# Kernel optimization log

Measured on AMD Instinct MI355X. Metric: run time of the kernel, lower is better.

Reference implementation:

```python
import jax, jax.numpy as jnp
import numpy as np

N_NODES = 50000
N_EDGES = 300000
IN_FEATS = 1433
HIDDEN = 16
OUT_FEATS = 7


def setup_inputs() -> dict:
    key = jax.random.key(0)
    k1, k2, k3, k4, k5, k6, k7, k8 = jax.random.split(key, 8)
    features = jax.random.normal(k1, (N_NODES, IN_FEATS), dtype=jnp.float32)
    src = jax.random.randint(k2, (N_EDGES,), 0, N_NODES, dtype=jnp.int32)
    dst = jax.random.randint(k3, (N_EDGES,), 0, N_NODES, dtype=jnp.int32)
    # Linear layer params (PyTorch default-ish init scale)
    s1 = 1.0 / np.sqrt(IN_FEATS)
    s2 = 1.0 / np.sqrt(HIDDEN)
    W1 = jax.random.uniform(k4, (IN_FEATS, HIDDEN), jnp.float32, -s1, s1)
    b1 = jax.random.uniform(k5, (HIDDEN,), jnp.float32, -s1, s1)
    W2 = jax.random.uniform(k6, (HIDDEN, OUT_FEATS), jnp.float32, -s2, s2)
    b2 = jax.random.uniform(k7, (OUT_FEATS,), jnp.float32, -s2, s2)
    return {"features": features, "src": src, "dst": dst,
            "W1": W1, "b1": b1, "W2": W2, "b2": b2}


def _gcn_layer(h, src, dst, W, b):
    # copy_src message + sum reduce + self term: h'_v = sum_{u->v} h_u + h_v
    agg = jax.ops.segment_sum(h[src], dst, num_segments=N_NODES) + h
    return agg @ W + b


def reference(features, src, dst, W1, b1, W2, b2):
    x = jax.nn.relu(_gcn_layer(features, src, dst, W1, b1))
    # dropout is identity in eval mode
    x = _gcn_layer(x, src, dst, W2, b2)
    return x
```

## Files before the change

kernel.cpp:

```cpp
#include <hip/hip_runtime.h>
#include <hip/hip_fp16.h>

#define N_NODES  50000
#define N_EDGES  300000
#define IN_FEATS 1433
#define HIDDEN   16
#define OUT_F    7
#define KPAD     1472
#define WROW     9

__global__ __launch_bounds__(256) void k1_gemm(
    const float* __restrict__ F, const float* __restrict__ W1,
    const float* __restrict__ b1, __half* __restrict__ H,
    __half* __restrict__ aggbuf)
{
    __shared__ unsigned int Wl[KPAD * WROW];
    const int tid = threadIdx.x;

    for (int idx = tid; idx < KPAD * 8; idx += 256) {
        int k = idx >> 3, c = idx & 7;
        unsigned int u = 0u;
        if (k < IN_FEATS) {
            __half2 h2 = __floats2half2_rn(W1[k * 16 + 2 * c], W1[k * 16 + 2 * c + 1]);
            u = *reinterpret_cast<unsigned int*>(&h2);
        }
        Wl[k * WROW + c] = u;
    }
    __syncthreads();

    const int lane = tid & 63;
    const float b1v = b1[lane & 15];
    const int gwave  = blockIdx.x * 4 + (tid >> 6);
    const int nwaves = gridDim.x * 4;

    for (int ch = gwave; ch < N_NODES / 4; ch += nwaves) {
        const int r0 = ch * 4;
        const float* fp = F + (size_t)r0 * IN_FEATS;

        float v[64];
        #pragma unroll
        for (int i = 0; i < 64; ++i) v[i] = 0.f;

        #pragma unroll 2
        for (int i = 0; i < 22; ++i) {
            const int k = i * 64 + lane;
            const float f0 = fp[k];
            const float f1 = fp[IN_FEATS + k];
            const float f2 = fp[2 * IN_FEATS + k];
            const float f3 = fp[3 * IN_FEATS + k];
            float wv[16];
            #pragma unroll
            for (int c = 0; c < 8; ++c) {
                unsigned int u = Wl[k * WROW + c];
                __half2 h2 = *reinterpret_cast<__half2*>(&u);
                float2 f = __half22float2(h2);
                wv[2 * c]     = f.x;
                wv[2 * c + 1] = f.y;
            }
            #pragma unroll
            for (int j = 0; j < 16; ++j) {
                v[j]      += f0 * wv[j];
                v[16 + j] += f1 * wv[j];
                v[32 + j] += f2 * wv[j];
                v[48 + j] += f3 * wv[j];
            }
        }
        {
            const int k = 1408 + lane;
            float f0 = 0.f, f1 = 0.f, f2 = 0.f, f3 = 0.f;
            if (k < IN_FEATS) {
                f0 = fp[k];
                f1 = fp[IN_FEATS + k];
                f2 = fp[2 * IN_FEATS + k];
                f3 = fp[3 * IN_FEATS + k];
            }
            float wv[16];
            #pragma unroll
            for (int c = 0; c < 8; ++c) {
                unsigned int u = Wl[k * WROW + c];
                __half2 h2 = *reinterpret_cast<__half2*>(&u);
                float2 f = __half22float2(h2);
                wv[2 * c]     = f.x;
                wv[2 * c + 1] = f.y;
            }
            #pragma unroll
            for (int j = 0; j < 16; ++j) {
                v[j]      += f0 * wv[j];
                v[16 + j] += f1 * wv[j];
                v[32 + j] += f2 * wv[j];
                v[48 + j] += f3 * wv[j];
            }
        }

        #pragma unroll
        for (int d = 5; d >= 0; --d) {
            const int half = 1 << d;
            const bool hi = (lane >> d) & 1;
            #pragma unroll
            for (int t = 0; t < (1 << d); ++t) {
                float sent = hi ? v[t] : v[t + half];
                float recv = __shfl_xor(sent, half, 64);
                float keep = hi ? v[t + half] : v[t];
                v[t] = keep + recv;
            }
        }
        const size_t off = (size_t)r0 * 16 + lane;
        H[off]      = __float2half(v[0]);
        aggbuf[off] = __float2half(v[0] + b1v);
    }
}

__global__ __launch_bounds__(256) void k2_scatter1(
    const int* __restrict__ src, const int* __restrict__ dst,
    const __half2* __restrict__ H2, __half2* __restrict__ agg2)
{
    int t = blockIdx.x * 256 + threadIdx.x;
    int e = t >> 3, p = t & 7;
    int s = src[e], d = dst[e];
    __half2 val = H2[(size_t)s * 8 + p];
    unsafeAtomicAdd(&agg2[(size_t)d * 8 + p], val);
}

__global__ __launch_bounds__(256) void k3_layer2(
    const __half2* __restrict__ agg2, const float* __restrict__ W2,
    const float* __restrict__ b2, float* __restrict__ G,
    float* __restrict__ out)
{
    int n = blockIdx.x * 256 + threadIdx.x;
    if (n >= N_NODES) return;
    float x[16];
    #pragma unroll
    for (int p = 0; p < 8; ++p) {
        float2 f = __half22float2(agg2[(size_t)n * 8 + p]);
        x[2 * p]     = f.x > 0.f ? f.x : 0.f;
        x[2 * p + 1] = f.y > 0.f ? f.y : 0.f;
    }
    #pragma unroll
    for (int j = 0; j < OUT_F; ++j) {
        float g = 0.f;
        #pragma unroll
        for (int k = 0; k < 16; ++k) g += x[k] * W2[k * OUT_F + j];
        G[(size_t)n * OUT_F + j] = g;
        out[(size_t)n * OUT_F + j] = g + b2[j];
    }
}

__global__ __launch_bounds__(256) void k4_scatter2(
    const int* __restrict__ src, const int* __restrict__ dst,
    const float* __restrict__ G, float* __restrict__ out)
{
    int t = blockIdx.x * 256 + threadIdx.x;
    int e = t / OUT_F, j = t % OUT_F;
    if (e < N_EDGES) {
        atomicAdd(&out[(size_t)dst[e] * OUT_F + j], G[(size_t)src[e] * OUT_F + j]);
    }
}

extern "C" void kernel_launch(void* const* d_in, const int* in_sizes, int n_in,
                              void* d_out, int out_size, void* d_ws, size_t ws_size,
                              hipStream_t stream)
{
    const float* F   = (const float*)d_in[0];
    const int*   src = (const int*)d_in[1];
    const int*   dst = (const int*)d_in[2];
    const float* W1  = (const float*)d_in[3];
    const float* b1  = (const float*)d_in[4];
    const float* W2  = (const float*)d_in[5];
    const float* b2  = (const float*)d_in[6];
    float* out = (float*)d_out;

    __half* H      = (__half*)d_ws;
    __half* aggbuf = H + (size_t)N_NODES * HIDDEN;
    float*  G      = (float*)(aggbuf + (size_t)N_NODES * HIDDEN);

    k1_gemm<<<768, 256, 0, stream>>>(F, W1, b1, H, aggbuf);
    k2_scatter1<<<(N_EDGES * 8) / 256, 256, 0, stream>>>(src, dst,
        (const __half2*)H, (__half2*)aggbuf);
    k3_layer2<<<(N_NODES + 255) / 256, 256, 0, stream>>>((const __half2*)aggbuf,
        W2, b2, G, out);
    k4_scatter2<<<(N_EDGES * OUT_F + 255) / 256, 256, 0, stream>>>(src, dst, G, out);
}
```

Baseline: 116.8 us.

## Pre-pack W1 to fp16 in global memory and launch one wave per row chunk

A new pre-kernel converts W1 to a packed fp16 array in the workspace. The GEMM kernel now reads weights directly from global/L2 with 16-byte vector loads instead of staging about 53KB of weights into LDS per block, which raised LDS use, cost a prologue and limited occupancy. The persistent grid-stride loop is replaced by one block per 16 rows (3125 blocks). The second scatter also switches to unsafeAtomicAdd for fp32 atomics. This adds an extra launch, and every wave re-reads the weights through cache.

```diff
diff --git a/kernel.cpp b/kernel.cpp
--- a/kernel.cpp
+++ b/kernel.cpp
@@ -7,107 +7,111 @@
 #define HIDDEN   16
 #define OUT_F    7
 #define KPAD     1472
-#define WROW     9
+
+__global__ __launch_bounds__(256) void k0_pack(
+    const float* __restrict__ W1, __half* __restrict__ Wp)
+{
+    int idx = blockIdx.x * 256 + threadIdx.x;
+    int k = idx >> 4, c = idx & 15;
+    float v = (k < IN_FEATS) ? W1[k * 16 + c] : 0.f;
+    Wp[idx] = __float2half(v);
+}
 
 __global__ __launch_bounds__(256) void k1_gemm(
-    const float* __restrict__ F, const float* __restrict__ W1,
+    const float* __restrict__ F, const __half* __restrict__ Wp,
     const float* __restrict__ b1, __half* __restrict__ H,
     __half* __restrict__ aggbuf)
 {
-    __shared__ unsigned int Wl[KPAD * WROW];
-    const int tid = threadIdx.x;
-
-    for (int idx = tid; idx < KPAD * 8; idx += 256) {
-        int k = idx >> 3, c = idx & 7;
-        unsigned int u = 0u;
-        if (k < IN_FEATS) {
-            __half2 h2 = __floats2half2_rn(W1[k * 16 + 2 * c], W1[k * 16 + 2 * c + 1]);
-            u = *reinterpret_cast<unsigned int*>(&h2);
-        }
-        Wl[k * WROW + c] = u;
-    }
-    __syncthreads();
-
+    const int tid  = threadIdx.x;
     const int lane = tid & 63;
     const float b1v = b1[lane & 15];
-    const int gwave  = blockIdx.x * 4 + (tid >> 6);
-    const int nwaves = gridDim.x * 4;
+    const int ch = blockIdx.x * 4 + (tid >> 6);
 
-    for (int ch = gwave; ch < N_NODES / 4; ch += nwaves) {
-        const int r0 = ch * 4;
-        const float* fp = F + (size_t)r0 * IN_FEATS;
+    const int r0 = ch * 4;
+    const float* fp = F + (size_t)r0 * IN_FEATS;
 
-        float v[64];
+    float v[64];
+    #pragma unroll
+    for (int i = 0; i < 64; ++i) v[i] = 0.f;
+
+    #pragma unroll 2
+    for (int i = 0; i < 22; ++i) {
+        const int k = i * 64 + lane;
+        const float f0 = fp[k];
+        const float f1 = fp[IN_FEATS + k];
+        const float f2 = fp[2 * IN_FEATS + k];
+        const float f3 = fp[3 * IN_FEATS + k];
+        const uint4* wrow = reinterpret_cast<const uint4*>(Wp + (size_t)k * 16);
+        const uint4 wa = wrow[0];
+        const uint4 wb = wrow[1];
+        float wv[16];
+        {
+            float2 t;
+            t = __half22float2(*(const __half2*)&wa.x); wv[0]=t.x;  wv[1]=t.y;
+            t = __half22float2(*(const __half2*)&wa.y); wv[2]=t.x;  wv[3]=t.y;
+            t = __half22float2(*(const __half2*)&wa.z); wv[4]=t.x;  wv[5]=t.y;
+            t = __half22float2(*(const __half2*)&wa.w); wv[6]=t.x;  wv[7]=t.y;
+            t = __half22float2(*(const __half2*)&wb.x); wv[8]=t.x;  wv[9]=t.y;
+            t = __half22float2(*(const __half2*)&wb.y); wv[10]=t.x; wv[11]=t.y;
+            t = __half22float2(*(const __half2*)&wb.z); wv[12]=t.x; wv[13]=t.y;
+            t = __half22float2(*(const __half2*)&wb.w); wv[14]=t.x; wv[15]=t.y;
+        }
         #pragma unroll
-        for (int i = 0; i < 64; ++i) v[i] = 0.f;
+        for (int j = 0; j < 16; ++j) {
+            v[j]      += f0 * wv[j];
+            v[16 + j] += f1 * wv[j];
+            v[32 + j] += f2 * wv[j];
+            v[48 + j] += f3 * wv[j];
+        }
+    }
+    {
+        const int k = 1408 + lane;
+        float f0 = 0.f, f1 = 0.f, f2 = 0.f, f3 = 0.f;
+        if (k < IN_FEATS) {
+            f0 = fp[k];
+            f1 = fp[IN_FEATS + k];
+            f2 = fp[2 * IN_FEATS + k];
+            f3 = fp[3 * IN_FEATS + k];
+        }
+        const uint4* wrow = reinterpret_cast<const uint4*>(Wp + (size_t)k * 16);
+        const uint4 wa = wrow[0];
+        const uint4 wb = wrow[1];
+        float wv[16];
+        {
+            float2 t;
+            t = __half22float2(*(const __half2*)&wa.x); wv[0]=t.x;  wv[1]=t.y;
+            t = __half22float2(*(const __half2*)&wa.y); wv[2]=t.x;  wv[3]=t.y;
+            t = __half22float2(*(const __half2*)&wa.z); wv[4]=t.x;  wv[5]=t.y;
+            t = __half22float2(*(const __half2*)&wa.w); wv[6]=t.x;  wv[7]=t.y;
+            t = __half22float2(*(const __half2*)&wb.x); wv[8]=t.x;  wv[9]=t.y;
+            t = __half22float2(*(const __half2*)&wb.y); wv[10]=t.x; wv[11]=t.y;
+            t = __half22float2(*(const __half2*)&wb.z); wv[12]=t.x; wv[13]=t.y;
+            t = __half22float2(*(const __half2*)&wb.w); wv[14]=t.x; wv[15]=t.y;
+        }
+        #pragma unroll
+        for (int j = 0; j < 16; ++j) {
+            v[j]      += f0 * wv[j];
+            v[16 + j] += f1 * wv[j];
+            v[32 + j] += f2 * wv[j];
+            v[48 + j] += f3 * wv[j];
+        }
+    }
 
-        #pragma unroll 2
-        for (int i = 0; i < 22; ++i) {
-            const int k = i * 64 + lane;
-            const float f0 = fp[k];
-            const float f1 = fp[IN_FEATS + k];
-            const float f2 = fp[2 * IN_FEATS + k];
-            const float f3 = fp[3 * IN_FEATS + k];
-            float wv[16];
-            #pragma unroll
-            for (int c = 0; c < 8; ++c) {
-                unsigned int u = Wl[k * WROW + c];
-                __half2 h2 = *reinterpret_cast<__half2*>(&u);
-                float2 f = __half22float2(h2);
-                wv[2 * c]     = f.x;
-                wv[2 * c + 1] = f.y;
-            }
-            #pragma unroll
-            for (int j = 0; j < 16; ++j) {
-                v[j]      += f0 * wv[j];
-                v[16 + j] += f1 * wv[j];
-                v[32 + j] += f2 * wv[j];
-                v[48 + j] += f3 * wv[j];
-            }
+    #pragma unroll
+    for (int d = 5; d >= 0; --d) {
+        const int half = 1 << d;
+        const bool hi = (lane >> d) & 1;
+        #pragma unroll
+        for (int t = 0; t < (1 << d); ++t) {
+            float sent = hi ? v[t] : v[t + half];
+            float recv = __shfl_xor(sent, half, 64);
+            float keep = hi ? v[t + half] : v[t];
+            v[t] = keep + recv;
         }
-        {
-            const int k = 1408 + lane;
-            float f0 = 0.f, f1 = 0.f, f2 = 0.f, f3 = 0.f;
-            if (k < IN_FEATS) {
-                f0 = fp[k];
-                f1 = fp[IN_FEATS + k];
-                f2 = fp[2 * IN_FEATS + k];
-                f3 = fp[3 * IN_FEATS + k];
-            }
-            float wv[16];
-            #pragma unroll
-            for (int c = 0; c < 8; ++c) {
-                unsigned int u = Wl[k * WROW + c];
-                __half2 h2 = *reinterpret_cast<__half2*>(&u);
-                float2 f = __half22float2(h2);
-                wv[2 * c]     = f.x;
-                wv[2 * c + 1] = f.y;
-            }
-            #pragma unroll
-            for (int j = 0; j < 16; ++j) {
-                v[j]      += f0 * wv[j];
-                v[16 + j] += f1 * wv[j];
-                v[32 + j] += f2 * wv[j];
-                v[48 + j] += f3 * wv[j];
-            }
-        }
-
-        #pragma unroll
-        for (int d = 5; d >= 0; --d) {
-            const int half = 1 << d;
-            const bool hi = (lane >> d) & 1;
-            #pragma unroll
-            for (int t = 0; t < (1 << d); ++t) {
-                float sent = hi ? v[t] : v[t + half];
-                float recv = __shfl_xor(sent, half, 64);
-                float keep = hi ? v[t + half] : v[t];
-                v[t] = keep + recv;
-            }
-        }
-        const size_t off = (size_t)r0 * 16 + lane;
-        H[off]      = __float2half(v[0]);
-        aggbuf[off] = __float2half(v[0] + b1v);
     }
+    const size_t off = (size_t)r0 * 16 + lane;
+    H[off]      = __float2half(v[0]);
+    aggbuf[off] = __float2half(v[0] + b1v);
 }
 
 __global__ __launch_bounds__(256) void k2_scatter1(
@@ -152,7 +156,8 @@
     int t = blockIdx.x * 256 + threadIdx.x;
     int e = t / OUT_F, j = t % OUT_F;
     if (e < N_EDGES) {
-        atomicAdd(&out[(size_t)dst[e] * OUT_F + j], G[(size_t)src[e] * OUT_F + j]);
+        unsafeAtomicAdd(&out[(size_t)dst[e] * OUT_F + j],
+                        G[(size_t)src[e] * OUT_F + j]);
     }
 }
 
@@ -172,8 +177,10 @@
     __half* H      = (__half*)d_ws;
     __half* aggbuf = H + (size_t)N_NODES * HIDDEN;
     float*  G      = (float*)(aggbuf + (size_t)N_NODES * HIDDEN);
+    __half* Wp     = (__half*)(G + (size_t)N_NODES * OUT_F);
 
-    k1_gemm<<<768, 256, 0, stream>>>(F, W1, b1, H, aggbuf);
+    k0_pack<<<(KPAD * 16) / 256, 256, 0, stream>>>(W1, Wp);
+    k1_gemm<<<N_NODES / 16, 256, 0, stream>>>(F, Wp, b1, H, aggbuf);
     k2_scatter1<<<(N_EDGES * 8) / 256, 256, 0, stream>>>(src, dst,
         (const __half2*)H, (__half2*)aggbuf);
     k3_layer2<<<(N_NODES + 255) / 256, 256, 0, stream>>>((const __half2*)aggbuf,
```

Result: no change. 116.9 us (+0.1%).

## Split layer-1 GEMM along K into non-persistent blocks with combine kernel

Applied to the files above, without the earlier changes.

Replaces the persistent layer-1 GEMM with a grid of short-lived blocks, each processing 16 rows over one half of the input dimension with half the LDS weight table, to raise occupancy and memory-level parallelism. Partial results go to two fp16 buffers that a new combine kernel sums with bias, and the scatter reads both halves. The cost is re-staging the weight slice in every block, an extra launch, and additional fp16 rounding of partials. The second scatter also switches to unsafe float atomics.

```diff
diff --git a/kernel.cpp b/kernel.cpp
--- a/kernel.cpp
+++ b/kernel.cpp
@@ -7,117 +7,130 @@
 #define HIDDEN   16
 #define OUT_F    7
 #define KPAD     1472
+#define KSPLIT   768
 #define WROW     9
 
-__global__ __launch_bounds__(256) void k1_gemm(
+__global__ __launch_bounds__(256, 5) void k1_gemm_half(
     const float* __restrict__ F, const float* __restrict__ W1,
-    const float* __restrict__ b1, __half* __restrict__ H,
-    __half* __restrict__ aggbuf)
+    __half* __restrict__ H0, __half* __restrict__ H1)
 {
-    __shared__ unsigned int Wl[KPAD * WROW];
-    const int tid = threadIdx.x;
+    __shared__ unsigned int Wl[KSPLIT * WROW];
+    const int tid    = threadIdx.x;
+    const int halfId = blockIdx.x & 1;
+    const int kbase  = halfId ? KSPLIT : 0;
+    const int nrows  = halfId ? (KPAD - KSPLIT) : KSPLIT;
 
-    for (int idx = tid; idx < KPAD * 8; idx += 256) {
-        int k = idx >> 3, c = idx & 7;
+    for (int idx = tid; idx < nrows * 8; idx += 256) {
+        int r = idx >> 3, c = idx & 7;
+        int k = kbase + r;
         unsigned int u = 0u;
         if (k < IN_FEATS) {
             __half2 h2 = __floats2half2_rn(W1[k * 16 + 2 * c], W1[k * 16 + 2 * c + 1]);
             u = *reinterpret_cast<unsigned int*>(&h2);
         }
-        Wl[k * WROW + c] = u;
+        Wl[r * WROW + c] = u;
     }
     __syncthreads();
 
     const int lane = tid & 63;
-    const float b1v = b1[lane & 15];
-    const int gwave  = blockIdx.x * 4 + (tid >> 6);
-    const int nwaves = gridDim.x * 4;
+    const int ch = (blockIdx.x >> 1) * 4 + (tid >> 6);
+    const int r0 = ch * 4;
+    const float* fp = F + (size_t)r0 * IN_FEATS + kbase;
 
-    for (int ch = gwave; ch < N_NODES / 4; ch += nwaves) {
-        const int r0 = ch * 4;
-        const float* fp = F + (size_t)r0 * IN_FEATS;
+    float v[64];
+    #pragma unroll
+    for (int i = 0; i < 64; ++i) v[i] = 0.f;
 
-        float v[64];
-        #pragma unroll
-        for (int i = 0; i < 64; ++i) v[i] = 0.f;
+    #define ITER_BODY(KL, M0, M1, M2, M3)                               \
+        {                                                               \
+            float wv[16];                                               \
+            _Pragma("unroll")                                           \
+            for (int c = 0; c < 8; ++c) {                               \
+                unsigned int u = Wl[(KL) * WROW + c];                   \
+                __half2 h2 = *reinterpret_cast<__half2*>(&u);           \
+                float2 f = __half22float2(h2);                          \
+                wv[2 * c]     = f.x;                                    \
+                wv[2 * c + 1] = f.y;                                    \
+            }                                                           \
+            _Pragma("unroll")                                           \
+            for (int j = 0; j < 16; ++j) {                              \
+                v[j]      += (M0) * wv[j];                              \
+                v[16 + j] += (M1) * wv[j];                              \
+                v[32 + j] += (M2) * wv[j];                              \
+                v[48 + j] += (M3) * wv[j];                              \
+            }                                                           \
+        }
 
+    if (halfId == 0) {
         #pragma unroll 2
-        for (int i = 0; i < 22; ++i) {
-            const int k = i * 64 + lane;
-            const float f0 = fp[k];
-            const float f1 = fp[IN_FEATS + k];
-            const float f2 = fp[2 * IN_FEATS + k];
-            const float f3 = fp[3 * IN_FEATS + k];
-            float wv[16];
-            #pragma unroll
-            for (int c = 0; c < 8; ++c) {
-                unsigned int u = Wl[k * WROW + c];
-                __half2 h2 = *reinterpret_cast<__half2*>(&u);
-                float2 f = __half22float2(h2);
-                wv[2 * c]     = f.x;
-                wv[2 * c + 1] = f.y;
-            }
-            #pragma unroll
-            for (int j = 0; j < 16; ++j) {
-                v[j]      += f0 * wv[j];
-                v[16 + j] += f1 * wv[j];
-                v[32 + j] += f2 * wv[j];
-                v[48 + j] += f3 * wv[j];
-            }
+        for (int i = 0; i < 12; ++i) {
+            const int kl = i * 64 + lane;
+            const float f0 = fp[kl];
+            const float f1 = fp[IN_FEATS + kl];
+            const float f2 = fp[2 * IN_FEATS + kl];
+            const float f3 = fp[3 * IN_FEATS + kl];
+            ITER_BODY(kl, f0, f1, f2, f3);
+        }
+    } else {
+        #pragma unroll 2
+        for (int i = 0; i < 10; ++i) {
+            const int kl = i * 64 + lane;
+            const float f0 = fp[kl];
+            const float f1 = fp[IN_FEATS + kl];
+            const float f2 = fp[2 * IN_FEATS + kl];
+            const float f3 = fp[3 * IN_FEATS + kl];
+            ITER_BODY(kl, f0, f1, f2, f3);
         }
         {
-            const int k = 1408 + lane;
-            float f0 = 0.f, f1 = 0.f, f2 = 0.f, f3 = 0.f;
-            if (k < IN_FEATS) {
-                f0 = fp[k];
-                f1 = fp[IN_FEATS + k];
-                f2 = fp[2 * IN_FEATS + k];
-                f3 = fp[3 * IN_FEATS + k];
-            }
-            float wv[16];
-            #pragma unroll
-            for (int c = 0; c < 8; ++c) {
-                unsigned int u = Wl[k * WROW + c];
-                __half2 h2 = *reinterpret_cast<__half2*>(&u);
-                float2 f = __half22float2(h2);
-                wv[2 * c]     = f.x;
-                wv[2 * c + 1] = f.y;
-            }
-            #pragma unroll
-            for (int j = 0; j < 16; ++j) {
-                v[j]      += f0 * wv[j];
-                v[16 + j] += f1 * wv[j];
-                v[32 + j] += f2 * wv[j];
-                v[48 + j] += f3 * wv[j];
-            }
+            const int kl = 640 + lane;
+            const bool m = (kbase + kl) < IN_FEATS;
+            const float f0 = m ? fp[kl] : 0.f;
+            const float f1 = m ? fp[IN_FEATS + kl] : 0.f;
+            const float f2 = m ? fp[2 * IN_FEATS + kl] : 0.f;
+            const float f3 = m ? fp[3 * IN_FEATS + kl] : 0.f;
+            ITER_BODY(kl, f0, f1, f2, f3);
         }
+    }
+    #undef ITER_BODY
 
+    #pragma unroll
+    for (int d = 5; d >= 0; --d) {
+        const int half = 1 << d;
+        const bool hi = (lane >> d) & 1;
         #pragma unroll
-        for (int d = 5; d >= 0; --d) {
-            const int half = 1 << d;
-            const bool hi = (lane >> d) & 1;
-            #pragma unroll
-            for (int t = 0; t < (1 << d); ++t) {
-                float sent = hi ? v[t] : v[t + half];
-                float recv = __shfl_xor(sent, half, 64);
-                float keep = hi ? v[t + half] : v[t];
-                v[t] = keep + recv;
-            }
+        for (int t = 0; t < (1 << d); ++t) {
+            float sent = hi ? v[t] : v[t + half];
+            float recv = __shfl_xor(sent, half, 64);
+            float keep = hi ? v[t + half] : v[t];
+            v[t] = keep + recv;
         }
-        const size_t off = (size_t)r0 * 16 + lane;
-        H[off]      = __float2half(v[0]);
-        aggbuf[off] = __float2half(v[0] + b1v);
     }
+    __half* Hout = halfId ? H1 : H0;
+    Hout[(size_t)r0 * 16 + lane] = __float2half(v[0]);
+}
+
+__global__ __launch_bounds__(256) void k1b_combine(
+    const __half2* __restrict__ H0, const __half2* __restrict__ H1,
+    const float* __restrict__ b1, __half2* __restrict__ agg2)
+{
+    int t = blockIdx.x * 256 + threadIdx.x;
+    if (t >= N_NODES * 8) return;
+    int p = t & 7;
+    float2 a = __half22float2(H0[t]);
+    float2 b = __half22float2(H1[t]);
+    agg2[t] = __floats2half2_rn(a.x + b.x + b1[2 * p],
+                                a.y + b.y + b1[2 * p + 1]);
 }
 
 __global__ __launch_bounds__(256) void k2_scatter1(
     const int* __restrict__ src, const int* __restrict__ dst,
-    const __half2* __restrict__ H2, __half2* __restrict__ agg2)
+    const __half2* __restrict__ H0, const __half2* __restrict__ H1,
+    __half2* __restrict__ agg2)
 {
     int t = blockIdx.x * 256 + threadIdx.x;
     int e = t >> 3, p = t & 7;
     int s = src[e], d = dst[e];
-    __half2 val = H2[(size_t)s * 8 + p];
+    __half2 val = __hadd2(H0[(size_t)s * 8 + p], H1[(size_t)s * 8 + p]);
     unsafeAtomicAdd(&agg2[(size_t)d * 8 + p], val);
 }
 
@@ -152,7 +165,8 @@
     int t = blockIdx.x * 256 + threadIdx.x;
     int e = t / OUT_F, j = t % OUT_F;
     if (e < N_EDGES) {
-        atomicAdd(&out[(size_t)dst[e] * OUT_F + j], G[(size_t)src[e] * OUT_F + j]);
+        unsafeAtomicAdd(&out[(size_t)dst[e] * OUT_F + j],
+                        G[(size_t)src[e] * OUT_F + j]);
     }
 }
 
@@ -169,13 +183,16 @@
     const float* b2  = (const float*)d_in[6];
     float* out = (float*)d_out;
 
-    __half* H      = (__half*)d_ws;
-    __half* aggbuf = H + (size_t)N_NODES * HIDDEN;
-    float*  G      = (float*)(aggbuf + (size_t)N_NODES * HIDDEN);
+    __half* H0     = (__half*)d_ws;
+    __half* H1     = H0 + (size_t)N_NODES * HIDDEN;
+    __half* aggbuf = H1 + (size_t)N_NODES * HIDDEN;
+    float*  G      = (float*)H0;
 
-    k1_gemm<<<768, 256, 0, stream>>>(F, W1, b1, H, aggbuf);
+    k1_gemm_half<<<6250, 256, 0, stream>>>(F, W1, H0, H1);
+    k1b_combine<<<(N_NODES * 8 + 255) / 256, 256, 0, stream>>>(
+        (const __half2*)H0, (const __half2*)H1, b1, (__half2*)aggbuf);
     k2_scatter1<<<(N_EDGES * 8) / 256, 256, 0, stream>>>(src, dst,
-        (const __half2*)H, (__half2*)aggbuf);
+        (const __half2*)H0, (const __half2*)H1, (__half2*)aggbuf);
     k3_layer2<<<(N_NODES + 255) / 256, 256, 0, stream>>>((const __half2*)aggbuf,
         W2, b2, G, out);
     k4_scatter2<<<(N_EDGES * OUT_F + 255) / 256, 256, 0, stream>>>(src, dst, G, out);
```

Measured after the change: 173.8 us. 48.9% more time.
